# Kernel optimization log

Hardware: AMD Instinct MI355X
Metric: run time of the kernel (lower is better)

The kernel has to match this reference:

```python
import jax, jax.numpy as jnp
import numpy as np

# ---- column/activation layout (matches transformer_info init kwarg) ----
N_COLS = 20          # continuous data columns
MODES = 50           # VGM modes per column (gumbel-softmax width)
SPAN = MODES + 1     # 1 tanh scalar + MODES gumbel logits
IN_DIM = 2048
OUT_DIM = N_COLS * SPAN  # 1020
TAU = 0.2
B = 16384
EPS = 1e-9

_spans = []
for i in range(N_COLS):
    st = i * SPAN
    _spans.append((st, st + 1, 0))          # tanh span (alpha)
    _spans.append((st + 1, st + SPAN, 1))   # gumbel-softmax span (beta/d)
N_SEG = len(_spans)

_seg = np.zeros(OUT_DIM, np.int32)   # segment id per output feature
_typ = np.zeros(OUT_DIM, np.int32)   # 0 = tanh, 1 = gumbel-softmax
for si, (s, e, t) in enumerate(_spans):
    _seg[s:e] = si
    _typ[s:e] = t
SEG = jnp.asarray(_seg)
TYP = jnp.asarray(_typ)


def setup_inputs() -> dict:
    key = jax.random.key(0)
    kx, kw, kb, ku = jax.random.split(key, 4)
    bound = 1.0 / np.sqrt(IN_DIM)  # init_bounded(dim=input_dim)
    x = jax.random.normal(kx, (B, IN_DIM), dtype=jnp.float32)
    W = jax.random.uniform(kw, (IN_DIM, OUT_DIM), minval=-bound, maxval=bound, dtype=jnp.float32)
    b = jax.random.uniform(kb, (OUT_DIM,), minval=-bound, maxval=bound, dtype=jnp.float32)
    u = jax.random.uniform(ku, (B, OUT_DIM), dtype=jnp.float32)  # uniform driving gumbel noise
    return {"x": x, "W": W, "b": b, "u": u}


def _segment_softmax(z):
    # softmax over each transformer_info span, fused via segment ops.
    zT = z.T  # [D, B]
    m = jax.ops.segment_max(zT, SEG, num_segments=N_SEG)      # [S, B]
    e = jnp.exp(zT - m[SEG])
    s = jax.ops.segment_sum(e, SEG, num_segments=N_SEG)       # [S, B]
    return (e / s[SEG]).T  # [B, D]


def reference(x, W, b, u):
    outputs = x @ W + b  # [B, OUT_DIM]
    # Gumbel(0,1) noise from uniform u
    g = -jnp.log(-jnp.log(jnp.clip(u, EPS, 1.0 - EPS)))
    soft = _segment_softmax((outputs + g) / TAU)
    # type 0 -> tanh, type 1 -> gumbel-softmax (single fused select)
    data_t = jnp.where(TYP == 0, jnp.tanh(outputs), soft)
    return outputs, data_t
```

## Files before the change

kernel.cpp:

```cpp
#include <hip/hip_runtime.h>
#include <stdint.h>

#define MDIM 16384
#define NDIM 1020
#define KDIM 2048
#define NPAD 1024
#define TK   (KDIM / 64)

typedef __attribute__((ext_vector_type(4))) float f32x4;
typedef __attribute__((ext_vector_type(8))) short short8;

#define MFMA16(a, b, c) __builtin_amdgcn_mfma_f32_16x16x32_bf16((a), (b), (c), 0, 0, 0)

template <int OFF>
static __device__ __forceinline__ short8 dsr(unsigned addr) {
    short8 r;
    asm volatile("ds_read_b128 %0, %1 offset:%2" : "=v"(r) : "v"(addr), "i"(OFF));
    return r;
}

__device__ __forceinline__ unsigned short f2bf(float f) {
    unsigned int u = __float_as_uint(f);
    unsigned int r = (u + 0x7FFFu + ((u >> 16) & 1u)) >> 16;
    return (unsigned short)r;
}

__global__ void prep_w_kernel(const float* __restrict__ W,
                              unsigned short* __restrict__ Wt) {
    const int id = blockIdx.x * 256 + threadIdx.x;
    const int n0 = (id & 255) * 4;
    const int k0 = (id >> 8) * 4;
    float a[4][4];
    if (n0 < NDIM) {
#pragma unroll
        for (int i = 0; i < 4; ++i) {
            const float* p = W + (size_t)(k0 + i) * NDIM + n0;
            a[i][0] = p[0]; a[i][1] = p[1]; a[i][2] = p[2]; a[i][3] = p[3];
        }
    } else {
#pragma unroll
        for (int i = 0; i < 4; ++i)
#pragma unroll
            for (int j = 0; j < 4; ++j) a[i][j] = 0.f;
    }
#pragma unroll
    for (int j = 0; j < 4; ++j) {
        uint2 p;
        p.x = (unsigned)f2bf(a[0][j]) | ((unsigned)f2bf(a[1][j]) << 16);
        p.y = (unsigned)f2bf(a[2][j]) | ((unsigned)f2bf(a[3][j]) << 16);
        *(uint2*)(Wt + (size_t)(n0 + j) * KDIM + k0) = p;
    }
}

__global__ void prep_x_kernel(const float* __restrict__ x,
                              unsigned short* __restrict__ Xb) {
    const size_t total = (size_t)MDIM * KDIM;
    const size_t stride = (size_t)gridDim.x * 256 * 8;
    for (size_t i = ((size_t)blockIdx.x * 256 + threadIdx.x) * 8; i < total; i += stride) {
        const float4 v0 = *(const float4*)(x + i);
        const float4 v1 = *(const float4*)(x + i + 4);
        uint4 p;
        p.x = (unsigned)f2bf(v0.x) | ((unsigned)f2bf(v0.y) << 16);
        p.y = (unsigned)f2bf(v0.z) | ((unsigned)f2bf(v0.w) << 16);
        p.z = (unsigned)f2bf(v1.x) | ((unsigned)f2bf(v1.y) << 16);
        p.w = (unsigned)f2bf(v1.z) | ((unsigned)f2bf(v1.w) << 16);
        *(uint4*)(Xb + i) = p;
    }
}

extern "C" __global__ __launch_bounds__(512, 2) void gemm8_kernel(
    const unsigned short* __restrict__ Xb,
    const unsigned short* __restrict__ Wt,
    const float* __restrict__ bias,
    float* __restrict__ out) {
    extern __shared__ unsigned short lds_raw[];

    const int tid  = threadIdx.x;
    const int lane = tid & 63;
    const int wid  = tid >> 6;
    const int wr   = wid >> 2;
    const int wc   = wid & 3;

    const int bid = blockIdx.x;
    const int swz = (bid & 7) * 32 + (bid >> 3);
    const int bm  = swz >> 2;
    const int bn  = swz & 3;

    const int srow = wid * 8 + (lane >> 3);
    const int scb  = ((lane & 7) ^ (lane >> 3)) * 8;
    const unsigned short* aS = Xb + (size_t)(bm * 256 + srow) * KDIM + scb;
    const unsigned short* bS = Wt + (size_t)(bn * 256 + srow) * KDIM + scb;

#define STAGE(BUFI, OP, STRIPE, S) do {                                          \
    const size_t ks_ = (size_t)(((S) * 64) & (KDIM - 1));                        \
    const unsigned short* sp_ =                                                  \
        ((OP) ? bS : aS) + (size_t)((STRIPE) * 64) * KDIM + ks_;                 \
    __builtin_amdgcn_global_load_lds(                                            \
        (const __attribute__((address_space(1))) unsigned int*)sp_,              \
        (__attribute__((address_space(3))) unsigned int*)(lds_raw +              \
            (BUFI) * 32768 + (OP) * 16384 + ((STRIPE) * 64 + wid * 8) * 64),     \
        16, 0, 0);                                                              \
} while (0)

#define VMCNT2 do {                                                             \
    asm volatile("s_waitcnt vmcnt(2)" ::: "memory");                            \
    __builtin_amdgcn_sched_barrier(0);                                          \
} while (0)

#define PH_TAIL                                                       \
    __builtin_amdgcn_s_barrier();                                     \
    asm volatile("s_waitcnt lgkmcnt(0)" ::: "memory");                \
    __builtin_amdgcn_sched_barrier(0);                                \
    __builtin_amdgcn_s_setprio(1);

#define PH_END                                                        \
    __builtin_amdgcn_sched_barrier(0);                                \
    __builtin_amdgcn_s_setprio(0);

#define MFMA32(MB, CUR)                                                         \
    _Pragma("unroll")                                                           \
    for (int k2 = 0; k2 < 2; ++k2)                                              \
        _Pragma("unroll")                                                       \
        for (int mi = 0; mi < 4; ++mi)                                          \
            _Pragma("unroll")                                                   \
            for (int nf = 0; nf < 4; ++nf)                                      \
                acc[(MB) + mi][nf] =                                            \
                    MFMA16(af[mi][k2], CUR[nf][k2], acc[(MB) + mi][nf]);

#define TILE(T, BUF, NB, CUR, NXT)                                              \
  {                                                      \
    af[0][0]=dsr<0*2048>(aA##BUF##_0); af[0][1]=dsr<0*2048>(aA##BUF##_1);       \
    af[1][0]=dsr<1*2048>(aA##BUF##_0); af[1][1]=dsr<1*2048>(aA##BUF##_1);       \
    af[2][0]=dsr<2*2048>(aA##BUF##_0); af[2][1]=dsr<2*2048>(aA##BUF##_1);       \
    af[3][0]=dsr<3*2048>(aA##BUF##_0); af[3][1]=dsr<3*2048>(aA##BUF##_1);       \
    NXT[0][0]=dsr<0*2048>(bB##NB##_0); NXT[0][1]=dsr<0*2048>(bB##NB##_1);       \
    NXT[1][0]=dsr<1*2048>(bB##NB##_0); NXT[1][1]=dsr<1*2048>(bB##NB##_1);       \
    STAGE(NB, 0, 1, (T) + 1); STAGE(NB, 0, 3, (T) + 1);                         \
    STAGE(BUF, 1, 0, (T) + 2); STAGE(BUF, 1, 1, (T) + 2);                       \
    PH_TAIL                                                                     \
    MFMA32(0, CUR)                                                              \
    PH_END                                                                      \
    __builtin_amdgcn_s_barrier();                                               \
                                                         \
    af[0][0]=dsr<4*2048>(aA##BUF##_0); af[0][1]=dsr<4*2048>(aA##BUF##_1);       \
    af[1][0]=dsr<5*2048>(aA##BUF##_0); af[1][1]=dsr<5*2048>(aA##BUF##_1);       \
    af[2][0]=dsr<6*2048>(aA##BUF##_0); af[2][1]=dsr<6*2048>(aA##BUF##_1);       \
    af[3][0]=dsr<7*2048>(aA##BUF##_0); af[3][1]=dsr<7*2048>(aA##BUF##_1);       \
    NXT[2][0]=dsr<2*2048>(bB##NB##_0); NXT[2][1]=dsr<2*2048>(bB##NB##_1);       \
    NXT[3][0]=dsr<3*2048>(bB##NB##_0); NXT[3][1]=dsr<3*2048>(bB##NB##_1);       \
    STAGE(BUF, 1, 2, (T) + 2); STAGE(BUF, 1, 3, (T) + 2);                       \
    STAGE(BUF, 0, 0, (T) + 2); STAGE(BUF, 0, 2, (T) + 2);                       \
    PH_TAIL                                                                     \
    MFMA32(4, CUR)                                                              \
    PH_END                                                                      \
    VMCNT2;                                                                     \
    __builtin_amdgcn_s_barrier();                                               \
  }

    const unsigned ldsbase =
        (unsigned)(uintptr_t)(__attribute__((address_space(3))) unsigned short*)lds_raw;
    const unsigned l15 = lane & 15, hi = lane >> 4, l7 = lane & 7;
    const unsigned c0 = (unsigned)((0 * 4 + hi) ^ l7) << 4;
    const unsigned c1 = (unsigned)((1 * 4 + hi) ^ l7) << 4;
    const unsigned pbA = ldsbase + (unsigned)(wr * 128 + l15) * 128;
    const unsigned pbB = ldsbase + 32768u + (unsigned)(wc * 64 + l15) * 128;
    const unsigned aA0_0 = pbA + c0,          aA0_1 = pbA + c1;
    const unsigned aA1_0 = pbA + 65536u + c0, aA1_1 = pbA + 65536u + c1;
    const unsigned bB0_0 = pbB + c0,          bB0_1 = pbB + c1;
    const unsigned bB1_0 = pbB + 65536u + c0, bB1_1 = pbB + 65536u + c1;

    f32x4 acc[8][4];
#pragma unroll
    for (int i = 0; i < 8; ++i)
#pragma unroll
        for (int j = 0; j < 4; ++j) {
            f32x4 z = {0.f, 0.f, 0.f, 0.f};
            acc[i][j] = z;
        }

    short8 af[4][2];
    short8 bfvP[4][2], bfvQ[4][2];

    STAGE(0, 0, 0, 0); STAGE(0, 0, 1, 0); STAGE(0, 0, 2, 0); STAGE(0, 0, 3, 0);
    STAGE(0, 1, 0, 0); STAGE(0, 1, 1, 0); STAGE(0, 1, 2, 0); STAGE(0, 1, 3, 0);
    STAGE(1, 1, 0, 1); STAGE(1, 1, 1, 1); STAGE(1, 1, 2, 1); STAGE(1, 1, 3, 1);
    STAGE(1, 0, 0, 1); STAGE(1, 0, 2, 1);
    VMCNT2;
    __builtin_amdgcn_s_barrier();

    bfvP[0][0]=dsr<0*2048>(bB0_0); bfvP[0][1]=dsr<0*2048>(bB0_1);
    bfvP[1][0]=dsr<1*2048>(bB0_0); bfvP[1][1]=dsr<1*2048>(bB0_1);
    bfvP[2][0]=dsr<2*2048>(bB0_0); bfvP[2][1]=dsr<2*2048>(bB0_1);
    bfvP[3][0]=dsr<3*2048>(bB0_0); bfvP[3][1]=dsr<3*2048>(bB0_1);
    asm volatile("s_waitcnt lgkmcnt(0)" ::: "memory");
    __builtin_amdgcn_sched_barrier(0);
    __builtin_amdgcn_s_barrier();

    for (int t2 = 0; t2 < TK; t2 += 2) {
        TILE(t2,     0, 1, bfvP, bfvQ)
        TILE(t2 + 1, 1, 0, bfvQ, bfvP)
    }

#pragma unroll
    for (int nf = 0; nf < 4; ++nf) {
        const int col = bn * 256 + wc * 64 + nf * 16 + (lane & 15);
        if (col < NDIM) {
            const float bv = bias[col];
#pragma unroll
            for (int mf = 0; mf < 8; ++mf) {
                const int row = bm * 256 + wr * 128 + mf * 16 + ((lane >> 4) << 2);
                float* op = out + (size_t)row * NDIM + col;
#pragma unroll
                for (int r = 0; r < 4; ++r)
                    op[(size_t)r * NDIM] = acc[mf][nf][r] + bv;
            }
        }
    }
#undef STAGE
#undef VMCNT2
#undef PH_TAIL
#undef PH_END
#undef MFMA32
#undef TILE
}

__global__ void gemm_bf_kernel(const unsigned short* __restrict__ Xb,
                               const unsigned short* __restrict__ Wt,
                               const float* __restrict__ bias,
                               float* __restrict__ out) {
    __shared__ __align__(16) unsigned short As[128][32];
    __shared__ __align__(16) unsigned short Bs[128][32];

    const int tid  = threadIdx.x;
    const int lane = tid & 63;
    const int wid  = tid >> 6;
    const int wr   = wid >> 1;
    const int wc   = wid & 1;
    const int bn   = blockIdx.x;
    const int bm   = blockIdx.y;

    f32x4 acc[4][4];
#pragma unroll
    for (int i = 0; i < 4; ++i)
#pragma unroll
        for (int j = 0; j < 4; ++j) {
            f32x4 z = {0.f, 0.f, 0.f, 0.f};
            acc[i][j] = z;
        }

    const unsigned short* abase =
        Xb + (size_t)(bm * 128 + wid * 16 + (lane >> 2)) * KDIM + (lane & 3) * 8;
    const unsigned short* bbase =
        Wt + (size_t)(bn * 128 + wid * 16 + (lane >> 2)) * KDIM + (lane & 3) * 8;

    for (int kt = 0; kt < KDIM; kt += 32) {
#pragma unroll
        for (int j = 0; j < 2; ++j)
            __builtin_amdgcn_global_load_lds(
                (const __attribute__((address_space(1))) unsigned int*)(abase + (size_t)j * 64 * KDIM + kt),
                (__attribute__((address_space(3))) unsigned int*)(&As[j * 64 + wid * 16][0]),
                16, 0, 0);
#pragma unroll
        for (int j = 0; j < 2; ++j)
            __builtin_amdgcn_global_load_lds(
                (const __attribute__((address_space(1))) unsigned int*)(bbase + (size_t)j * 64 * KDIM + kt),
                (__attribute__((address_space(3))) unsigned int*)(&Bs[j * 64 + wid * 16][0]),
                16, 0, 0);
        __syncthreads();

        short8 af[4], bfr[4];
#pragma unroll
        for (int mi = 0; mi < 4; ++mi)
            af[mi] = *(const short8*)&As[wr * 64 + mi * 16 + (lane & 15)][(lane >> 4) * 8];
#pragma unroll
        for (int ni = 0; ni < 4; ++ni)
            bfr[ni] = *(const short8*)&Bs[wc * 64 + ni * 16 + (lane & 15)][(lane >> 4) * 8];

#pragma unroll
        for (int mi = 0; mi < 4; ++mi)
#pragma unroll
            for (int ni = 0; ni < 4; ++ni)
                acc[mi][ni] = MFMA16(af[mi], bfr[ni], acc[mi][ni]);

        __syncthreads();
    }

#pragma unroll
    for (int ni = 0; ni < 4; ++ni) {
        const int col = bn * 128 + wc * 64 + ni * 16 + (lane & 15);
        if (col < NDIM) {
            const float bv = bias[col];
#pragma unroll
            for (int mi = 0; mi < 4; ++mi) {
                const int row = bm * 128 + wr * 64 + mi * 16 + ((lane >> 4) << 2);
                float* op = out + (size_t)row * NDIM + col;
#pragma unroll
                for (int r = 0; r < 4; ++r)
                    op[(size_t)r * NDIM] = acc[mi][ni][r] + bv;
            }
        }
    }
}

__global__ void act_kernel(const float* __restrict__ outp,
                           const float* __restrict__ u,
                           float* __restrict__ dt) {
    const int lane  = threadIdx.x & 63;
    const int gwave = (blockIdx.x * 256 + threadIdx.x) >> 6;
    const int nwave = gridDim.x * 4;
    const int total = MDIM * 20;
    const float NEG_INF = -__builtin_inff();

    for (int unit = gwave; unit < total; unit += nwave) {
        const int row = unit / 20;
        const int sp  = unit - row * 20;
        const size_t base = (size_t)row * NDIM + sp * 51;

        float o = 0.f, uu = 0.5f;
        if (lane < 51) {
            o  = outp[base + lane];
            uu = u[base + lane];
        }
        const bool soft = (lane >= 1) && (lane < 51);

        const float uc = fmaxf(uu, 1e-9f);
        const float g  = -__logf(-__logf(uc));
        float z = soft ? (o + g) * 5.0f : NEG_INF;

        float m = z;
#pragma unroll
        for (int off = 32; off; off >>= 1) m = fmaxf(m, __shfl_xor(m, off));
        float e = soft ? __expf(z - m) : 0.f;
        float s = e;
#pragma unroll
        for (int off = 32; off; off >>= 1) s += __shfl_xor(s, off);

        float res;
        if (lane == 0) {
            const float ex = __expf(-2.0f * fabsf(o));
            const float t  = (1.0f - ex) / (1.0f + ex);
            res = copysignf(t, o);
        } else {
            res = e / s;
        }
        if (lane < 51) dt[base + lane] = res;
    }
}

extern "C" void kernel_launch(void* const* d_in, const int* in_sizes, int n_in,
                              void* d_out, int out_size, void* d_ws, size_t ws_size,
                              hipStream_t stream) {
    const float* x = (const float*)d_in[0];
    const float* W = (const float*)d_in[1];
    const float* b = (const float*)d_in[2];
    const float* u = (const float*)d_in[3];
    float* out = (float*)d_out;
    float* dt  = out + (size_t)MDIM * NDIM;
    unsigned short* Wt = (unsigned short*)d_ws;
    unsigned short* Xb = Wt + (size_t)NPAD * KDIM;

    prep_w_kernel<<<512, 256, 0, stream>>>(W, Wt);
    prep_x_kernel<<<2048, 256, 0, stream>>>(x, Xb);

    const hipError_t attr_ok = hipFuncSetAttribute(
        (const void*)gemm8_kernel, hipFuncAttributeMaxDynamicSharedMemorySize, 131072);
    if (attr_ok == hipSuccess) {
        gemm8_kernel<<<256, 512, 131072, stream>>>(Xb, Wt, b, out);
    } else {
        gemm_bf_kernel<<<dim3(8, 128), 256, 0, stream>>>(Xb, Wt, b, out);
    }

    act_kernel<<<8192, 256, 0, stream>>>(out, u, dt);
}
```

Measured before the change: 205.5 us.

## Restructure GEMM main loop with fine-grained lgkmcnt waits and end-of-tile staging

```diff
diff --git a/kernel.cpp b/kernel.cpp
--- a/kernel.cpp
+++ b/kernel.cpp
@@ -18,6 +18,10 @@
     asm volatile("ds_read_b128 %0, %1 offset:%2" : "=v"(r) : "v"(addr), "i"(OFF));
     return r;
 }
+
+#define LGKM(N)                                                       \
+    asm volatile("s_waitcnt lgkmcnt(" #N ")" ::: "memory");           \
+    __builtin_amdgcn_sched_barrier(0);
 
 __device__ __forceinline__ unsigned short f2bf(float f) {
     unsigned int u = __float_as_uint(f);
@@ -102,61 +106,6 @@
         16, 0, 0);                                                              \
 } while (0)
 
-#define VMCNT2 do {                                                             \
-    asm volatile("s_waitcnt vmcnt(2)" ::: "memory");                            \
-    __builtin_amdgcn_sched_barrier(0);                                          \
-} while (0)
-
-#define PH_TAIL                                                       \
-    __builtin_amdgcn_s_barrier();                                     \
-    asm volatile("s_waitcnt lgkmcnt(0)" ::: "memory");                \
-    __builtin_amdgcn_sched_barrier(0);                                \
-    __builtin_amdgcn_s_setprio(1);
-
-#define PH_END                                                        \
-    __builtin_amdgcn_sched_barrier(0);                                \
-    __builtin_amdgcn_s_setprio(0);
-
-#define MFMA32(MB, CUR)                                                         \
-    _Pragma("unroll")                                                           \
-    for (int k2 = 0; k2 < 2; ++k2)                                              \
-        _Pragma("unroll")                                                       \
-        for (int mi = 0; mi < 4; ++mi)                                          \
-            _Pragma("unroll")                                                   \
-            for (int nf = 0; nf < 4; ++nf)                                      \
-                acc[(MB) + mi][nf] =                                            \
-                    MFMA16(af[mi][k2], CUR[nf][k2], acc[(MB) + mi][nf]);
-
-#define TILE(T, BUF, NB, CUR, NXT)                                              \
-  {                                                      \
-    af[0][0]=dsr<0*2048>(aA##BUF##_0); af[0][1]=dsr<0*2048>(aA##BUF##_1);       \
-    af[1][0]=dsr<1*2048>(aA##BUF##_0); af[1][1]=dsr<1*2048>(aA##BUF##_1);       \
-    af[2][0]=dsr<2*2048>(aA##BUF##_0); af[2][1]=dsr<2*2048>(aA##BUF##_1);       \
-    af[3][0]=dsr<3*2048>(aA##BUF##_0); af[3][1]=dsr<3*2048>(aA##BUF##_1);       \
-    NXT[0][0]=dsr<0*2048>(bB##NB##_0); NXT[0][1]=dsr<0*2048>(bB##NB##_1);       \
-    NXT[1][0]=dsr<1*2048>(bB##NB##_0); NXT[1][1]=dsr<1*2048>(bB##NB##_1);       \
-    STAGE(NB, 0, 1, (T) + 1); STAGE(NB, 0, 3, (T) + 1);                         \
-    STAGE(BUF, 1, 0, (T) + 2); STAGE(BUF, 1, 1, (T) + 2);                       \
-    PH_TAIL                                                                     \
-    MFMA32(0, CUR)                                                              \
-    PH_END                                                                      \
-    __builtin_amdgcn_s_barrier();                                               \
-                                                         \
-    af[0][0]=dsr<4*2048>(aA##BUF##_0); af[0][1]=dsr<4*2048>(aA##BUF##_1);       \
-    af[1][0]=dsr<5*2048>(aA##BUF##_0); af[1][1]=dsr<5*2048>(aA##BUF##_1);       \
-    af[2][0]=dsr<6*2048>(aA##BUF##_0); af[2][1]=dsr<6*2048>(aA##BUF##_1);       \
-    af[3][0]=dsr<7*2048>(aA##BUF##_0); af[3][1]=dsr<7*2048>(aA##BUF##_1);       \
-    NXT[2][0]=dsr<2*2048>(bB##NB##_0); NXT[2][1]=dsr<2*2048>(bB##NB##_1);       \
-    NXT[3][0]=dsr<3*2048>(bB##NB##_0); NXT[3][1]=dsr<3*2048>(bB##NB##_1);       \
-    STAGE(BUF, 1, 2, (T) + 2); STAGE(BUF, 1, 3, (T) + 2);                       \
-    STAGE(BUF, 0, 0, (T) + 2); STAGE(BUF, 0, 2, (T) + 2);                       \
-    PH_TAIL                                                                     \
-    MFMA32(4, CUR)                                                              \
-    PH_END                                                                      \
-    VMCNT2;                                                                     \
-    __builtin_amdgcn_s_barrier();                                               \
-  }
-
     const unsigned ldsbase =
         (unsigned)(uintptr_t)(__attribute__((address_space(3))) unsigned short*)lds_raw;
     const unsigned l15 = lane & 15, hi = lane >> 4, l7 = lane & 7;
@@ -178,27 +127,59 @@
             acc[i][j] = z;
         }
 
-    short8 af[4][2];
-    short8 bfvP[4][2], bfvQ[4][2];
+    short8 af0[8], af1[8];
+    short8 bfv[4][2];
+
+#define RB(BUF, K)                                                    \
+    bfv[0][K] = dsr<0 * 2048>(bB##BUF##_##K);                         \
+    bfv[1][K] = dsr<1 * 2048>(bB##BUF##_##K);                         \
+    bfv[2][K] = dsr<2 * 2048>(bB##BUF##_##K);                         \
+    bfv[3][K] = dsr<3 * 2048>(bB##BUF##_##K);
+
+#define RA(BUF, K, MF) af##K[MF] = dsr<(MF) * 2048>(aA##BUF##_##K);
+
+#define G(K, MF, LG)                                                  \
+    LGKM(LG)                                                          \
+    __builtin_amdgcn_s_setprio(1);                                    \
+    acc[MF][0] = MFMA16(af##K[MF], bfv[0][K], acc[MF][0]);            \
+    acc[MF][1] = MFMA16(af##K[MF], bfv[1][K], acc[MF][1]);            \
+    acc[MF][2] = MFMA16(af##K[MF], bfv[2][K], acc[MF][2]);            \
+    acc[MF][3] = MFMA16(af##K[MF], bfv[3][K], acc[MF][3]);            \
+    __builtin_amdgcn_s_setprio(0);
+
+#define TILE(T, BUF)                                                            \
+  {                                                                             \
+    RB(BUF, 0)                                                  \
+    RA(BUF, 0, 0) RA(BUF, 0, 1) RA(BUF, 0, 2) RA(BUF, 0, 3)                     \
+    RA(BUF, 0, 4) RA(BUF, 0, 5) RA(BUF, 0, 6) RA(BUF, 0, 7)       \
+    RB(BUF, 1)                                                  \
+    G(0, 0, 11) G(0, 1, 10) G(0, 2, 9) G(0, 3, 8) G(0, 4, 7) G(0, 5, 6)         \
+    RA(BUF, 1, 0) RA(BUF, 1, 1) RA(BUF, 1, 2) RA(BUF, 1, 3)                     \
+    RA(BUF, 1, 4) RA(BUF, 1, 5) RA(BUF, 1, 6) RA(BUF, 1, 7)      \
+    G(0, 6, 13) G(0, 7, 12)                                                     \
+    G(1, 0, 7) G(1, 1, 6) G(1, 2, 5) G(1, 3, 4)                                 \
+    G(1, 4, 3) G(1, 5, 2) G(1, 6, 1) G(1, 7, 0)                                 \
+    __builtin_amdgcn_s_barrier();        \
+    STAGE(BUF, 0, 0, (T) + 2); STAGE(BUF, 0, 1, (T) + 2);                       \
+    STAGE(BUF, 0, 2, (T) + 2); STAGE(BUF, 0, 3, (T) + 2);                       \
+    STAGE(BUF, 1, 0, (T) + 2); STAGE(BUF, 1, 1, (T) + 2);                       \
+    STAGE(BUF, 1, 2, (T) + 2); STAGE(BUF, 1, 3, (T) + 2);                       \
+    asm volatile("s_waitcnt vmcnt(8)" ::: "memory");      \
+    __builtin_amdgcn_sched_barrier(0);                                          \
+    __builtin_amdgcn_s_barrier();                                               \
+  }
 
     STAGE(0, 0, 0, 0); STAGE(0, 0, 1, 0); STAGE(0, 0, 2, 0); STAGE(0, 0, 3, 0);
     STAGE(0, 1, 0, 0); STAGE(0, 1, 1, 0); STAGE(0, 1, 2, 0); STAGE(0, 1, 3, 0);
+    STAGE(1, 0, 0, 1); STAGE(1, 0, 1, 1); STAGE(1, 0, 2, 1); STAGE(1, 0, 3, 1);
     STAGE(1, 1, 0, 1); STAGE(1, 1, 1, 1); STAGE(1, 1, 2, 1); STAGE(1, 1, 3, 1);
-    STAGE(1, 0, 0, 1); STAGE(1, 0, 2, 1);
-    VMCNT2;
-    __builtin_amdgcn_s_barrier();
-
-    bfvP[0][0]=dsr<0*2048>(bB0_0); bfvP[0][1]=dsr<0*2048>(bB0_1);
-    bfvP[1][0]=dsr<1*2048>(bB0_0); bfvP[1][1]=dsr<1*2048>(bB0_1);
-    bfvP[2][0]=dsr<2*2048>(bB0_0); bfvP[2][1]=dsr<2*2048>(bB0_1);
-    bfvP[3][0]=dsr<3*2048>(bB0_0); bfvP[3][1]=dsr<3*2048>(bB0_1);
-    asm volatile("s_waitcnt lgkmcnt(0)" ::: "memory");
+    asm volatile("s_waitcnt vmcnt(8)" ::: "memory");
     __builtin_amdgcn_sched_barrier(0);
     __builtin_amdgcn_s_barrier();
 
     for (int t2 = 0; t2 < TK; t2 += 2) {
-        TILE(t2,     0, 1, bfvP, bfvQ)
-        TILE(t2 + 1, 1, 0, bfvQ, bfvP)
+        TILE(t2, 0)
+        TILE(t2 + 1, 1)
     }
 
 #pragma unroll
@@ -217,10 +198,9 @@
         }
     }
 #undef STAGE
-#undef VMCNT2
-#undef PH_TAIL
-#undef PH_END
-#undef MFMA32
+#undef RB
+#undef RA
+#undef G
 #undef TILE
 }
 
```

Result: faster. 194.6 us (-5.3%).

## Fuse fp32-to-bf16 conversion of x into GEMM mainloop via register staging

Applied to the files above, without the earlier changes.

```diff
diff --git a/kernel.cpp b/kernel.cpp
--- a/kernel.cpp
+++ b/kernel.cpp
@@ -17,6 +17,16 @@
     short8 r;
     asm volatile("ds_read_b128 %0, %1 offset:%2" : "=v"(r) : "v"(addr), "i"(OFF));
     return r;
+}
+template <int OFF>
+static __device__ __forceinline__ void dsw64(unsigned addr, uint2 v) {
+    asm volatile("ds_write_b64 %0, %1 offset:%2" :: "v"(addr), "v"(v), "i"(OFF));
+}
+
+__device__ __forceinline__ unsigned packbf(float lo, float hi) {
+    const unsigned r0 = __float_as_uint(lo) + 0x8000u;
+    const unsigned r1 = __float_as_uint(hi) + 0x8000u;
+    return __builtin_amdgcn_perm(r1, r0, 0x07060302u);
 }
 
 __device__ __forceinline__ unsigned short f2bf(float f) {
@@ -68,8 +78,8 @@
     }
 }
 
-extern "C" __global__ __launch_bounds__(512, 2) void gemm8_kernel(
-    const unsigned short* __restrict__ Xb,
+extern "C" __global__ __launch_bounds__(512, 2) void gemm10_kernel(
+    const float* __restrict__ x,
     const unsigned short* __restrict__ Wt,
     const float* __restrict__ bias,
     float* __restrict__ out) {
@@ -88,77 +98,52 @@
 
     const int srow = wid * 8 + (lane >> 3);
     const int scb  = ((lane & 7) ^ (lane >> 3)) * 8;
-    const unsigned short* aS = Xb + (size_t)(bm * 256 + srow) * KDIM + scb;
     const unsigned short* bS = Wt + (size_t)(bn * 256 + srow) * KDIM + scb;
 
-#define STAGE(BUFI, OP, STRIPE, S) do {                                          \
-    const size_t ks_ = (size_t)(((S) * 64) & (KDIM - 1));                        \
+#define STAGEB(BUFI, STRIPE, S) do {                                             \
     const unsigned short* sp_ =                                                  \
-        ((OP) ? bS : aS) + (size_t)((STRIPE) * 64) * KDIM + ks_;                 \
+        bS + (size_t)((STRIPE) * 64) * KDIM + (size_t)(((S) & 31) * 64);         \
     __builtin_amdgcn_global_load_lds(                                            \
         (const __attribute__((address_space(1))) unsigned int*)sp_,              \
         (__attribute__((address_space(3))) unsigned int*)(lds_raw +              \
-            (BUFI) * 32768 + (OP) * 16384 + ((STRIPE) * 64 + wid * 8) * 64),     \
-        16, 0, 0);                                                              \
+            (BUFI) * 32768 + 16384 + ((STRIPE) * 64 + wid * 8) * 64),            \
+        16, 0, 0);                                                               \
 } while (0)
 
-#define VMCNT2 do {                                                             \
-    asm volatile("s_waitcnt vmcnt(2)" ::: "memory");                            \
-    __builtin_amdgcn_sched_barrier(0);                                          \
-} while (0)
-
-#define PH_TAIL                                                       \
-    __builtin_amdgcn_s_barrier();                                     \
-    asm volatile("s_waitcnt lgkmcnt(0)" ::: "memory");                \
-    __builtin_amdgcn_sched_barrier(0);                                \
-    __builtin_amdgcn_s_setprio(1);
-
-#define PH_END                                                        \
-    __builtin_amdgcn_sched_barrier(0);                                \
-    __builtin_amdgcn_s_setprio(0);
-
-#define MFMA32(MB, CUR)                                                         \
-    _Pragma("unroll")                                                           \
-    for (int k2 = 0; k2 < 2; ++k2)                                              \
-        _Pragma("unroll")                                                       \
-        for (int mi = 0; mi < 4; ++mi)                                          \
-            _Pragma("unroll")                                                   \
-            for (int nf = 0; nf < 4; ++nf)                                      \
-                acc[(MB) + mi][nf] =                                            \
-                    MFMA16(af[mi][k2], CUR[nf][k2], acc[(MB) + mi][nf]);
-
-#define TILE(T, BUF, NB, CUR, NXT)                                              \
-  {                                                      \
-    af[0][0]=dsr<0*2048>(aA##BUF##_0); af[0][1]=dsr<0*2048>(aA##BUF##_1);       \
-    af[1][0]=dsr<1*2048>(aA##BUF##_0); af[1][1]=dsr<1*2048>(aA##BUF##_1);       \
-    af[2][0]=dsr<2*2048>(aA##BUF##_0); af[2][1]=dsr<2*2048>(aA##BUF##_1);       \
-    af[3][0]=dsr<3*2048>(aA##BUF##_0); af[3][1]=dsr<3*2048>(aA##BUF##_1);       \
-    NXT[0][0]=dsr<0*2048>(bB##NB##_0); NXT[0][1]=dsr<0*2048>(bB##NB##_1);       \
-    NXT[1][0]=dsr<1*2048>(bB##NB##_0); NXT[1][1]=dsr<1*2048>(bB##NB##_1);       \
-    STAGE(NB, 0, 1, (T) + 1); STAGE(NB, 0, 3, (T) + 1);                         \
-    STAGE(BUF, 1, 0, (T) + 2); STAGE(BUF, 1, 1, (T) + 2);                       \
-    PH_TAIL                                                                     \
-    MFMA32(0, CUR)                                                              \
-    PH_END                                                                      \
-    __builtin_amdgcn_s_barrier();                                               \
-                                                         \
-    af[0][0]=dsr<4*2048>(aA##BUF##_0); af[0][1]=dsr<4*2048>(aA##BUF##_1);       \
-    af[1][0]=dsr<5*2048>(aA##BUF##_0); af[1][1]=dsr<5*2048>(aA##BUF##_1);       \
-    af[2][0]=dsr<6*2048>(aA##BUF##_0); af[2][1]=dsr<6*2048>(aA##BUF##_1);       \
-    af[3][0]=dsr<7*2048>(aA##BUF##_0); af[3][1]=dsr<7*2048>(aA##BUF##_1);       \
-    NXT[2][0]=dsr<2*2048>(bB##NB##_0); NXT[2][1]=dsr<2*2048>(bB##NB##_1);       \
-    NXT[3][0]=dsr<3*2048>(bB##NB##_0); NXT[3][1]=dsr<3*2048>(bB##NB##_1);       \
-    STAGE(BUF, 1, 2, (T) + 2); STAGE(BUF, 1, 3, (T) + 2);                       \
-    STAGE(BUF, 0, 0, (T) + 2); STAGE(BUF, 0, 2, (T) + 2);                       \
-    PH_TAIL                                                                     \
-    MFMA32(4, CUR)                                                              \
-    PH_END                                                                      \
-    VMCNT2;                                                                     \
-    __builtin_amdgcn_s_barrier();                                               \
-  }
+    const int h = lane >> 4, g = lane & 15;
+    const float* aF = x + (size_t)(bm * 256 + wid * 32 + h) * KDIM + g * 4;
 
     const unsigned ldsbase =
         (unsigned)(uintptr_t)(__attribute__((address_space(3))) unsigned short*)lds_raw;
+    const unsigned awbE =
+        ldsbase + (unsigned)(wid * 32 + h) * 128 +
+        ((unsigned)((g >> 1) ^ h) << 4) + (unsigned)(g & 1) * 8;
+    const unsigned awbO  = awbE ^ 0x40u;
+    const unsigned awb0E = awbE,           awb0O = awbO;
+    const unsigned awb1E = awbE + 65536u,  awb1O = awbO + 65536u;
+
+    float4 av[8];
+#define AGLD(T) {                                                     \
+    const float* ap_ = aF + (size_t)(((T) & 31) * 64);                \
+    av[0] = *(const float4*)(ap_);                                    \
+    av[1] = *(const float4*)(ap_ + 4 * KDIM);                         \
+    av[2] = *(const float4*)(ap_ + 8 * KDIM);                         \
+    av[3] = *(const float4*)(ap_ + 12 * KDIM);                        \
+    av[4] = *(const float4*)(ap_ + 16 * KDIM);                        \
+    av[5] = *(const float4*)(ap_ + 20 * KDIM);                        \
+    av[6] = *(const float4*)(ap_ + 24 * KDIM);                        \
+    av[7] = *(const float4*)(ap_ + 28 * KDIM);                        \
+}
+#define CVT1(AWE, AWO, I)                                             \
+    { uint2 v_;                                                       \
+      v_.x = packbf(av[I].x, av[I].y);                                \
+      v_.y = packbf(av[I].z, av[I].w);                                \
+      dsw64<(I) * 512>(((I) & 1) ? (AWO) : (AWE), v_); }
+#define CVTW(AWE, AWO)                                                \
+    CVT1(AWE, AWO, 0) CVT1(AWE, AWO, 1) CVT1(AWE, AWO, 2)             \
+    CVT1(AWE, AWO, 3) CVT1(AWE, AWO, 4) CVT1(AWE, AWO, 5)             \
+    CVT1(AWE, AWO, 6) CVT1(AWE, AWO, 7)
+
     const unsigned l15 = lane & 15, hi = lane >> 4, l7 = lane & 7;
     const unsigned c0 = (unsigned)((0 * 4 + hi) ^ l7) << 4;
     const unsigned c1 = (unsigned)((1 * 4 + hi) ^ l7) << 4;
@@ -178,27 +163,78 @@
             acc[i][j] = z;
         }
 
-    short8 af[4][2];
-    short8 bfvP[4][2], bfvQ[4][2];
-
-    STAGE(0, 0, 0, 0); STAGE(0, 0, 1, 0); STAGE(0, 0, 2, 0); STAGE(0, 0, 3, 0);
-    STAGE(0, 1, 0, 0); STAGE(0, 1, 1, 0); STAGE(0, 1, 2, 0); STAGE(0, 1, 3, 0);
-    STAGE(1, 1, 0, 1); STAGE(1, 1, 1, 1); STAGE(1, 1, 2, 1); STAGE(1, 1, 3, 1);
-    STAGE(1, 0, 0, 1); STAGE(1, 0, 2, 1);
-    VMCNT2;
-    __builtin_amdgcn_s_barrier();
-
-    bfvP[0][0]=dsr<0*2048>(bB0_0); bfvP[0][1]=dsr<0*2048>(bB0_1);
-    bfvP[1][0]=dsr<1*2048>(bB0_0); bfvP[1][1]=dsr<1*2048>(bB0_1);
-    bfvP[2][0]=dsr<2*2048>(bB0_0); bfvP[2][1]=dsr<2*2048>(bB0_1);
-    bfvP[3][0]=dsr<3*2048>(bB0_0); bfvP[3][1]=dsr<3*2048>(bB0_1);
+#define PH_TAIL                                                       \
+    __builtin_amdgcn_s_barrier();                                     \
+    asm volatile("s_waitcnt lgkmcnt(0)" ::: "memory");                \
+    __builtin_amdgcn_sched_barrier(0);                                \
+    __builtin_amdgcn_s_setprio(1);
+
+#define PH_MFMA(MF0)                                                  \
+    _Pragma("unroll")                                                 \
+    for (int nf = 0; nf < 4; ++nf) {                                  \
+        acc[MF0][nf]     = MFMA16(af0[0], bfv[nf][0], acc[MF0][nf]);      \
+        acc[MF0][nf]     = MFMA16(af0[1], bfv[nf][1], acc[MF0][nf]);      \
+        acc[MF0 + 1][nf] = MFMA16(af1[0], bfv[nf][0], acc[MF0 + 1][nf]);  \
+        acc[MF0 + 1][nf] = MFMA16(af1[1], bfv[nf][1], acc[MF0 + 1][nf]);  \
+    }                                                                 \
+    __builtin_amdgcn_sched_barrier(0);                                \
+    __builtin_amdgcn_s_setprio(0);
+
+#define RDA(BUF, MF0)                                                 \
+    af0[0] = dsr<(MF0) * 2048>(aA##BUF##_0);                          \
+    af0[1] = dsr<(MF0) * 2048>(aA##BUF##_1);                          \
+    af1[0] = dsr<(MF0) * 2048 + 2048>(aA##BUF##_0);                   \
+    af1[1] = dsr<(MF0) * 2048 + 2048>(aA##BUF##_1);
+
+#define RDB(BUF, NF)                                                  \
+    bfv[NF][0] = dsr<(NF) * 2048>(bB##BUF##_0);                       \
+    bfv[NF][1] = dsr<(NF) * 2048>(bB##BUF##_1);
+
+#define TILE(T, BUF, NB, AWE, AWO)                                              \
+  {                                                                             \
+    short8 bfv[4][2];                                                           \
+    short8 af0[2], af1[2];                                                      \
+              \
+    RDB(BUF, 0) RDB(BUF, 1) RDB(BUF, 2) RDB(BUF, 3)                             \
+    RDA(BUF, 0)                                                                 \
+    AGLD((T) + 1)                                                               \
+    PH_TAIL                                                                     \
+    PH_MFMA(0)                                                                  \
+    __builtin_amdgcn_s_barrier();                                               \
+                                                         \
+    RDA(BUF, 2)                                                                 \
+    STAGEB(NB, 0, (T) + 1); STAGEB(NB, 1, (T) + 1);                             \
+    PH_TAIL                                                                     \
+    PH_MFMA(2)                                                                  \
+    __builtin_amdgcn_s_barrier();                                               \
+                                                         \
+    RDA(BUF, 4)                                                                 \
+    STAGEB(NB, 2, (T) + 1); STAGEB(NB, 3, (T) + 1);                             \
+    PH_TAIL                                                                     \
+    PH_MFMA(4)                                                                  \
+    __builtin_amdgcn_s_barrier();                                               \
+       \
+    RDA(BUF, 6)                                                                 \
+    CVTW(AWE, AWO)                                                              \
+    PH_TAIL                                                                     \
+    PH_MFMA(6)                                                                  \
+    asm volatile("s_waitcnt vmcnt(0)" ::: "memory");                            \
+    __builtin_amdgcn_sched_barrier(0);                                          \
+    __builtin_amdgcn_s_barrier();                                               \
+  }
+
+    AGLD(0)
+    STAGEB(0, 0, 0); STAGEB(0, 1, 0); STAGEB(0, 2, 0); STAGEB(0, 3, 0);
+    CVTW(awb0E, awb0O)
     asm volatile("s_waitcnt lgkmcnt(0)" ::: "memory");
     __builtin_amdgcn_sched_barrier(0);
+    asm volatile("s_waitcnt vmcnt(0)" ::: "memory");
+    __builtin_amdgcn_sched_barrier(0);
     __builtin_amdgcn_s_barrier();
 
     for (int t2 = 0; t2 < TK; t2 += 2) {
-        TILE(t2,     0, 1, bfvP, bfvQ)
-        TILE(t2 + 1, 1, 0, bfvQ, bfvP)
+        TILE(t2,     0, 1, awb1E, awb1O)
+        TILE(t2 + 1, 1, 0, awb0E, awb0O)
     }
 
 #pragma unroll
@@ -216,11 +252,14 @@
             }
         }
     }
-#undef STAGE
-#undef VMCNT2
+#undef STAGEB
+#undef AGLD
+#undef CVT1
+#undef CVTW
 #undef PH_TAIL
-#undef PH_END
-#undef MFMA32
+#undef PH_MFMA
+#undef RDA
+#undef RDB
 #undef TILE
 }
 
@@ -360,13 +399,13 @@
     unsigned short* Xb = Wt + (size_t)NPAD * KDIM;
 
     prep_w_kernel<<<512, 256, 0, stream>>>(W, Wt);
-    prep_x_kernel<<<2048, 256, 0, stream>>>(x, Xb);
 
     const hipError_t attr_ok = hipFuncSetAttribute(
-        (const void*)gemm8_kernel, hipFuncAttributeMaxDynamicSharedMemorySize, 131072);
+        (const void*)gemm10_kernel, hipFuncAttributeMaxDynamicSharedMemorySize, 131072);
     if (attr_ok == hipSuccess) {
-        gemm8_kernel<<<256, 512, 131072, stream>>>(Xb, Wt, b, out);
+        gemm10_kernel<<<256, 512, 131072, stream>>>(x, Wt, b, out);
     } else {
+        prep_x_kernel<<<2048, 256, 0, stream>>>(x, Xb);
         gemm_bf_kernel<<<dim3(8, 128), 256, 0, stream>>>(Xb, Wt, b, out);
     }
 
```

After: 183.4 us, median of 4. -10.8%, faster.
